# Performance work log

Hardware: AMD Instinct MI355X
Metric: run time of the kernel (lower is better)

The kernel has to match this reference:

```python
import jax, jax.numpy as jnp
import numpy as np
import math

D_MODEL = 1024
NUM_HEADS = 16
HEAD_DIM = D_MODEL // NUM_HEADS
REPETITIONS = 3
NEG = -10000.0


def setup_inputs() -> dict:
    key = jax.random.key(0)
    ks = jax.random.split(key, 5)
    B, S = 2, 2048
    x = jax.random.normal(ks[0], (B, S, D_MODEL), dtype=jnp.float32)
    Wqkv_w = jax.random.normal(ks[1], (3 * D_MODEL, D_MODEL), dtype=jnp.float32) * (1.0 / math.sqrt(D_MODEL))
    Wqkv_b = jax.random.normal(ks[2], (3 * D_MODEL,), dtype=jnp.float32) * 0.02
    out_w = jax.random.normal(ks[3], (D_MODEL, D_MODEL), dtype=jnp.float32) * (1.0 / math.sqrt(D_MODEL))
    out_b = jax.random.normal(ks[4], (D_MODEL,), dtype=jnp.float32) * 0.02
    return {"x": x, "Wqkv_w": Wqkv_w, "Wqkv_b": Wqkv_b, "out_w": out_w, "out_b": out_b}


def _self_attention(q, k, v, mask):
    # q,k,v: (B,S,H,D); mask: (S,S) additive causal (-10000 above diagonal)
    scale = 1.0 / math.sqrt(q.shape[-1])
    scores = jnp.einsum('bthd,bshd->bhts', q, k * scale) + mask  # (B,H,S,S)
    attn = jax.nn.softmax(scores, axis=-1)
    return jnp.einsum('bhts,bshd->bthd', attn, v)  # (B,S,H,D)


def reference(x, Wqkv_w, Wqkv_b, out_w, out_b):
    B, S, _ = x.shape
    qkv = x @ Wqkv_w.T + Wqkv_b                       # (B,S,3*D_MODEL)
    qkv = qkv.reshape(B, S, 3, NUM_HEADS, HEAD_DIM)
    q, k, v = qkv[:, :, 0], qkv[:, :, 1], qkv[:, :, 2]
    mask = jnp.triu(jnp.full((S, S), NEG, dtype=x.dtype), 1)
    context = _self_attention(q, k, v, mask)
    # recurrent re-attention: rep_dim == 'q' -> query replaced by previous context
    for _ in range(REPETITIONS - 1):
        context = _self_attention(context, k, v, mask)
    out = context.reshape(B, S, D_MODEL) @ out_w.T + out_b
    return out
```

## Files before the change

kernel.cpp:

```cpp
#include <hip/hip_runtime.h>


#define D_MODEL 1024
#define NHEADS  16
#define HD      64
#define SEQ     2048
#define BATCH   2
#define NROWS   (BATCH*SEQ)
#define NQKV    (3*D_MODEL)
#define SCL2F   0.1803368801111601f
#define MASK2   (-14426.950408889634f)

typedef __bf16 bf16x8 __attribute__((ext_vector_type(8)));
typedef float  f32x4  __attribute__((ext_vector_type(4)));
typedef unsigned short us8 __attribute__((ext_vector_type(8)));
typedef unsigned short us4 __attribute__((ext_vector_type(4)));
typedef short  s16x4  __attribute__((ext_vector_type(4)));

__device__ __forceinline__ unsigned short f2bf(float f) {
  unsigned int u = __float_as_uint(f);
  u = (u + 0x7fffu + ((u >> 16) & 1u)) >> 16;
  return (unsigned short)u;
}

union Pack8 { us8 v; unsigned short e[8]; };
union Pack4 { us4 v; unsigned short e[4]; };

__device__ __forceinline__ us8 cvt8(const float4 &a, const float4 &b) {
  Pack8 p;
  p.e[0]=f2bf(a.x); p.e[1]=f2bf(a.y); p.e[2]=f2bf(a.z); p.e[3]=f2bf(a.w);
  p.e[4]=f2bf(b.x); p.e[5]=f2bf(b.y); p.e[6]=f2bf(b.z); p.e[7]=f2bf(b.w);
  return p.v;
}

__device__ __forceinline__ void gl_lds16(const unsigned short* g, unsigned short* l) {
  __builtin_amdgcn_global_load_lds(
      (const __attribute__((address_space(1))) unsigned int*)g,
      (__attribute__((address_space(3))) unsigned int*)l, 16, 0, 0);
}

#define CVT_N1 (NROWS*D_MODEL)
#define CVT_N2 (NQKV*D_MODEL)
#define CVT_N3 (D_MODEL*D_MODEL)

__global__ __launch_bounds__(256) void cvt_all(
    const float* __restrict__ x, const float* __restrict__ wq,
    const float* __restrict__ ow,
    unsigned short* __restrict__ xb, unsigned short* __restrict__ wqb,
    unsigned short* __restrict__ owb)
{
  size_t i = ((size_t)blockIdx.x * 256 + threadIdx.x) * 8;
  const float* src; unsigned short* dst; size_t off;
  if (i < CVT_N1)                { src = x;  dst = xb;  off = i; }
  else if (i < CVT_N1 + CVT_N2)  { src = wq; dst = wqb; off = i - CVT_N1; }
  else                           { src = ow; dst = owb; off = i - CVT_N1 - CVT_N2; }
  float4 a = *(const float4*)(src + off);
  float4 b = *(const float4*)(src + off + 4);
  *(us8*)(dst + off) = cvt8(a, b);
}

__global__ __launch_bounds__(256) void qkv_gemm(
    const unsigned short* __restrict__ xb, const unsigned short* __restrict__ wqb,
    const float* __restrict__ bias,
    unsigned short* __restrict__ q, unsigned short* __restrict__ k,
    unsigned short* __restrict__ vT)
{
  __shared__ __align__(16) unsigned short As[128*64];
  __shared__ __align__(16) unsigned short Bs[128*64];
  const int tid = threadIdx.x;
  const int m0 = blockIdx.y * 128, n0 = blockIdx.x * 128;
  const int wave = tid >> 6, lane = tid & 63;
  const int wm = (wave >> 1) * 64, wn = (wave & 1) * 64;
  const int lrow = lane & 15, quad = lane >> 4;

  const int dr = lane >> 3;
  const int pg = lane & 7;
  const int sg = (pg ^ dr) * 8;
  const unsigned short* gA[4]; const unsigned short* gB[4];
  unsigned short *lA[4], *lB[4];
  #pragma unroll
  for (int i = 0; i < 4; i++) {
    int c = wave*4 + i;
    gA[i] = xb  + (size_t)(m0 + c*8 + dr) * D_MODEL + sg;
    gB[i] = wqb + (size_t)(n0 + c*8 + dr) * D_MODEL + sg;
    lA[i] = &As[c*512];
    lB[i] = &Bs[c*512];
  }
  const int px0 = (quad ^ (lrow & 7)) * 8;
  const int px1 = ((quad + 4) ^ (lrow & 7)) * 8;

  f32x4 acc[4][4];
  #pragma unroll
  for (int i = 0; i < 4; i++)
    #pragma unroll
    for (int j = 0; j < 4; j++) acc[i][j] = (f32x4){0.f,0.f,0.f,0.f};

  for (int k0 = 0; k0 < D_MODEL; k0 += 64) {
    __syncthreads();
    #pragma unroll
    for (int i = 0; i < 4; i++) { gl_lds16(gA[i] + k0, lA[i]); gl_lds16(gB[i] + k0, lB[i]); }
    __syncthreads();
    bf16x8 af[4][2], bfr[4][2];
    #pragma unroll
    for (int mf = 0; mf < 4; mf++) {
      int row = wm + mf*16 + lrow;
      af[mf][0] = *(const bf16x8*)&As[row*64 + px0];
      af[mf][1] = *(const bf16x8*)&As[row*64 + px1];
    }
    #pragma unroll
    for (int nb = 0; nb < 4; nb++) {
      int row = wn + nb*16 + lrow;
      bfr[nb][0] = *(const bf16x8*)&Bs[row*64 + px0];
      bfr[nb][1] = *(const bf16x8*)&Bs[row*64 + px1];
    }
    #pragma unroll
    for (int h = 0; h < 2; h++)
      #pragma unroll
      for (int mf = 0; mf < 4; mf++)
        #pragma unroll
        for (int nb = 0; nb < 4; nb++)
          acc[mf][nb] = __builtin_amdgcn_mfma_f32_16x16x32_bf16(af[mf][h], bfr[nb][h], acc[mf][nb], 0, 0, 0);
  }

  #pragma unroll
  for (int mf = 0; mf < 4; mf++) {
    #pragma unroll
    for (int nb = 0; nb < 4; nb++) {
      int n = n0 + wn + nb*16 + lrow;
      int which = n >> 10;
      int h  = (n >> 6) & 15;
      int hd = n & 63;
      int mb = m0 + wm + mf*16 + quad*4;
      int b  = mb >> 11;
      int s  = mb & 2047;
      float bi = bias[n];
      if (which == 2) {
        Pack4 p4;
        #pragma unroll
        for (int r = 0; r < 4; r++) p4.e[r] = f2bf(acc[mf][nb][r] + bi);
        *(us4*)&vT[((size_t)((b*NHEADS + h)*HD + hd))*SEQ + s] = p4.v;
      } else {
        unsigned short* dst = (which == 0) ? q : k;
        float scl = (which == 0) ? SCL2F : 1.0f;
        #pragma unroll
        for (int r = 0; r < 4; r++)
          dst[(size_t)((b*NHEADS + h)*SEQ + s + r)*HD + hd] = f2bf((acc[mf][nb][r] + bi) * scl);
      }
    }
  }
}

#define LDQ 72

__global__ __launch_bounds__(256) void attn3(
    const unsigned short* __restrict__ qg,
    const unsigned short* __restrict__ kg,
    const unsigned short* __restrict__ vTg,
    unsigned short* __restrict__ ctx)
{
  __shared__ __align__(16) unsigned short Ks[4][64*LDQ];
  __shared__ __align__(16) unsigned short Vs[4][64*LDQ];
  unsigned short* QC = &Vs[0][0];

  const int tid  = threadIdx.x;
  const int w    = tid >> 6, lane = tid & 63;
  const int lrow = lane & 15, quad = lane >> 4;
  const int bh = blockIdx.x;
  const int yy = blockIdx.y;
  const int base = (blockIdx.x + yy) & 7;
  const int qt = (yy < 8) ? base : (15 - base);
  const unsigned short* qbase = qg  + (size_t)bh * SEQ * HD;
  const unsigned short* kbase = kg  + (size_t)bh * SEQ * HD;
  const unsigned short* vbase = vTg + (size_t)bh * HD * SEQ;
  unsigned short* cbase = ctx + (size_t)bh * SEQ * HD;

  const int srow = tid >> 2;
  const int sco  = (tid & 3) * 16;
  const int qrow = tid >> 1, qc0 = (tid & 1) * 32;

  {
    const unsigned short* src = qbase + (size_t)(qt*128 + qrow)*HD + qc0;
    *(uint4*)&QC[qrow*LDQ + qc0]      = *(const uint4*)src;
    *(uint4*)&QC[qrow*LDQ + qc0 + 8]  = *(const uint4*)(src + 8);
    *(uint4*)&QC[qrow*LDQ + qc0 + 16] = *(const uint4*)(src + 16);
    *(uint4*)&QC[qrow*LDQ + qc0 + 24] = *(const uint4*)(src + 24);
  }
  __syncthreads();

  bf16x8 qb[2][2];
  #pragma unroll
  for (int qgi = 0; qgi < 2; qgi++) {
    qb[qgi][0] = *(const bf16x8*)&QC[(w*32 + qgi*16 + lrow)*LDQ + quad*8];
    qb[qgi][1] = *(const bf16x8*)&QC[(w*32 + qgi*16 + lrow)*LDQ + 32 + quad*8];
  }
  __syncthreads();

  const int qwbase = qt*128 + w*32;
  const int npair = qt + 1;

  for (int rep = 0; rep < 3; ++rep) {
    f32x4 od[2][4];
    #pragma unroll
    for (int qgi = 0; qgi < 2; qgi++)
      #pragma unroll
      for (int df = 0; df < 4; df++) od[qgi][df] = (f32x4){0.f,0.f,0.f,0.f};
    float ls[2] = {0.f, 0.f};

    uint4 ka0, ka1, kb0, kb1, va0, va1, vb0, vb1;
    {
      const unsigned short* ks = kbase + (size_t)srow*HD + sco;
      ka0 = *(const uint4*)ks;  ka1 = *(const uint4*)(ks + 8);
      kb0 = *(const uint4*)(ks + 64*HD);  kb1 = *(const uint4*)(ks + 64*HD + 8);
      const unsigned short* vs = vbase + (size_t)srow*SEQ + sco;
      va0 = *(const uint4*)vs;  va1 = *(const uint4*)(vs + 8);
      vb0 = *(const uint4*)(vs + 64);  vb1 = *(const uint4*)(vs + 64 + 8);
    }

    for (int t = 0; t < npair; ++t) {
      const int pb = (t & 1) * 2;
      *(uint4*)&Ks[pb][srow*LDQ + sco]       = ka0;
      *(uint4*)&Ks[pb][srow*LDQ + sco + 8]   = ka1;
      *(uint4*)&Ks[pb+1][srow*LDQ + sco]     = kb0;
      *(uint4*)&Ks[pb+1][srow*LDQ + sco + 8] = kb1;
      *(uint4*)&Vs[pb][srow*LDQ + sco]       = va0;
      *(uint4*)&Vs[pb][srow*LDQ + sco + 8]   = va1;
      *(uint4*)&Vs[pb+1][srow*LDQ + sco]     = vb0;
      *(uint4*)&Vs[pb+1][srow*LDQ + sco + 8] = vb1;
      if (t + 1 < npair) {
        const unsigned short* ks = kbase + (size_t)((2*t+2)*64 + srow)*HD + sco;
        ka0 = *(const uint4*)ks;  ka1 = *(const uint4*)(ks + 8);
        kb0 = *(const uint4*)(ks + 64*HD);  kb1 = *(const uint4*)(ks + 64*HD + 8);
        const unsigned short* vs = vbase + (size_t)srow*SEQ + (2*t+2)*64 + sco;
        va0 = *(const uint4*)vs;  va1 = *(const uint4*)(vs + 8);
        vb0 = *(const uint4*)(vs + 64);  vb1 = *(const uint4*)(vs + 64 + 8);
      }
      __syncthreads();

      #pragma unroll
      for (int half = 0; half < 2; ++half) {
        const int bb = pb + half;
        const int sbase = (2*t + half) * 64;
        if (sbase > qwbase + 31) continue;
        f32x4 sc[2][4];
        #pragma unroll
        for (int sf = 0; sf < 4; sf++) {
          bf16x8 a0 = *(const bf16x8*)&Ks[bb][(sf*16 + lrow)*LDQ + quad*8];
          bf16x8 a1 = *(const bf16x8*)&Ks[bb][(sf*16 + lrow)*LDQ + 32 + quad*8];
          f32x4 z0 = (f32x4){0.f,0.f,0.f,0.f}, z1 = z0;
          z0 = __builtin_amdgcn_mfma_f32_16x16x32_bf16(a0, qb[0][0], z0, 0, 0, 0);
          z1 = __builtin_amdgcn_mfma_f32_16x16x32_bf16(a0, qb[1][0], z1, 0, 0, 0);
          z0 = __builtin_amdgcn_mfma_f32_16x16x32_bf16(a1, qb[0][1], z0, 0, 0, 0);
          z1 = __builtin_amdgcn_mfma_f32_16x16x32_bf16(a1, qb[1][1], z1, 0, 0, 0);
          sc[0][sf] = z0; sc[1][sf] = z1;
        }
        if (sbase + 63 > qwbase) {
          #pragma unroll
          for (int qgi = 0; qgi < 2; qgi++) {
            int ql = qwbase + qgi*16 + lrow;
            #pragma unroll
            for (int sf = 0; sf < 4; sf++)
              #pragma unroll
              for (int r = 0; r < 4; r++)
                if (sbase + sf*16 + quad*4 + r > ql) sc[qgi][sf][r] += MASK2;
          }
        }
        s16x4 pf[2][4];
        #pragma unroll
        for (int qgi = 0; qgi < 2; qgi++) {
          float lp = 0.f;
          #pragma unroll
          for (int sf = 0; sf < 4; sf++) {
            Pack4 pk;
            #pragma unroll
            for (int r = 0; r < 4; r++) {
              float pe = __builtin_amdgcn_exp2f(sc[qgi][sf][r]);
              lp += pe;
              pk.e[r] = __builtin_bit_cast(unsigned short, (__bf16)pe);
            }
            pf[qgi][sf] = __builtin_bit_cast(s16x4, pk.v);
          }
          ls[qgi] += lp;
        }
        #pragma unroll
        for (int df = 0; df < 4; df++) {
          s16x4 v0 = *(const s16x4*)&Vs[bb][(df*16 + lrow)*LDQ +  0 + quad*4];
          s16x4 v1 = *(const s16x4*)&Vs[bb][(df*16 + lrow)*LDQ + 16 + quad*4];
          s16x4 v2 = *(const s16x4*)&Vs[bb][(df*16 + lrow)*LDQ + 32 + quad*4];
          s16x4 v3 = *(const s16x4*)&Vs[bb][(df*16 + lrow)*LDQ + 48 + quad*4];
          od[0][df] = __builtin_amdgcn_mfma_f32_16x16x16bf16_1k(v0, pf[0][0], od[0][df], 0, 0, 0);
          od[1][df] = __builtin_amdgcn_mfma_f32_16x16x16bf16_1k(v0, pf[1][0], od[1][df], 0, 0, 0);
          od[0][df] = __builtin_amdgcn_mfma_f32_16x16x16bf16_1k(v1, pf[0][1], od[0][df], 0, 0, 0);
          od[1][df] = __builtin_amdgcn_mfma_f32_16x16x16bf16_1k(v1, pf[1][1], od[1][df], 0, 0, 0);
          od[0][df] = __builtin_amdgcn_mfma_f32_16x16x16bf16_1k(v2, pf[0][2], od[0][df], 0, 0, 0);
          od[1][df] = __builtin_amdgcn_mfma_f32_16x16x16bf16_1k(v2, pf[1][2], od[1][df], 0, 0, 0);
          od[0][df] = __builtin_amdgcn_mfma_f32_16x16x16bf16_1k(v3, pf[0][3], od[0][df], 0, 0, 0);
          od[1][df] = __builtin_amdgcn_mfma_f32_16x16x16bf16_1k(v3, pf[1][3], od[1][df], 0, 0, 0);
        }
      }
    }

    #pragma unroll
    for (int qgi = 0; qgi < 2; qgi++) {
      ls[qgi] += __shfl_xor(ls[qgi], 16);
      ls[qgi] += __shfl_xor(ls[qgi], 32);
    }

    __syncthreads();
    #pragma unroll
    for (int qgi = 0; qgi < 2; qgi++) {
      float f = ((rep < 2) ? SCL2F : 1.0f) / ls[qgi];
      #pragma unroll
      for (int df = 0; df < 4; df++) {
        Pack4 pk;
        #pragma unroll
        for (int r = 0; r < 4; r++)
          pk.e[r] = __builtin_bit_cast(unsigned short, (__bf16)(od[qgi][df][r] * f));
        *(us4*)&QC[(w*32 + qgi*16 + lrow)*LDQ + df*16 + quad*4] = pk.v;
      }
    }
    __syncthreads();
    if (rep < 2) {
      #pragma unroll
      for (int qgi = 0; qgi < 2; qgi++) {
        qb[qgi][0] = *(const bf16x8*)&QC[(w*32 + qgi*16 + lrow)*LDQ + quad*8];
        qb[qgi][1] = *(const bf16x8*)&QC[(w*32 + qgi*16 + lrow)*LDQ + 32 + quad*8];
      }
      __syncthreads();
    }
  }

  {
    unsigned short* dst = cbase + (size_t)(qt*128 + qrow)*HD + qc0;
    *(uint4*)dst        = *(const uint4*)&QC[qrow*LDQ + qc0];
    *(uint4*)(dst + 8)  = *(const uint4*)&QC[qrow*LDQ + qc0 + 8];
    *(uint4*)(dst + 16) = *(const uint4*)&QC[qrow*LDQ + qc0 + 16];
    *(uint4*)(dst + 24) = *(const uint4*)&QC[qrow*LDQ + qc0 + 24];
  }
}

__global__ __launch_bounds__(256) void out_gemm(
    const unsigned short* __restrict__ ctx, const unsigned short* __restrict__ owb,
    const float* __restrict__ bias, float* __restrict__ out)
{
  __shared__ __align__(16) unsigned short As[128*64];
  __shared__ __align__(16) unsigned short Bs[64*64];
  const int tid = threadIdx.x;
  const int m0 = blockIdx.y * 128, n0 = blockIdx.x * 64;
  const int wave = tid >> 6, lane = tid & 63;
  const int wm = (wave >> 1) * 64, wn = (wave & 1) * 32;
  const int lrow = lane & 15, quad = lane >> 4;

  const int dr = lane >> 3, pg = lane & 7;
  const int sg = (pg ^ dr) * 8;
  size_t aoff[4]; unsigned short* lA[4];
  #pragma unroll
  for (int i = 0; i < 4; i++) {
    int c = wave*4 + i;
    int row = m0 + c*8 + dr;
    aoff[i] = ((size_t)((row >> 11)*NHEADS)*SEQ + (row & 2047))*HD + sg;
    lA[i] = &As[c*512];
  }
  const unsigned short* gB[2]; unsigned short* lB[2];
  #pragma unroll
  for (int j = 0; j < 2; j++) {
    int c = wave*2 + j;
    gB[j] = owb + (size_t)(n0 + c*8 + dr) * D_MODEL + sg;
    lB[j] = &Bs[c*512];
  }
  const int px0 = (quad ^ (lrow & 7)) * 8;
  const int px1 = ((quad + 4) ^ (lrow & 7)) * 8;

  f32x4 acc[4][2];
  #pragma unroll
  for (int i = 0; i < 4; i++)
    #pragma unroll
    for (int j = 0; j < 2; j++) acc[i][j] = (f32x4){0.f,0.f,0.f,0.f};

  for (int k0 = 0; k0 < D_MODEL; k0 += 64) {
    size_t hoff = (size_t)(k0 >> 6) * SEQ * HD;
    __syncthreads();
    #pragma unroll
    for (int i = 0; i < 4; i++) gl_lds16(ctx + aoff[i] + hoff, lA[i]);
    #pragma unroll
    for (int j = 0; j < 2; j++) gl_lds16(gB[j] + k0, lB[j]);
    __syncthreads();
    bf16x8 af[4][2], bfr[2][2];
    #pragma unroll
    for (int mf = 0; mf < 4; mf++) {
      int row = wm + mf*16 + lrow;
      af[mf][0] = *(const bf16x8*)&As[row*64 + px0];
      af[mf][1] = *(const bf16x8*)&As[row*64 + px1];
    }
    #pragma unroll
    for (int nb = 0; nb < 2; nb++) {
      int row = wn + nb*16 + lrow;
      bfr[nb][0] = *(const bf16x8*)&Bs[row*64 + px0];
      bfr[nb][1] = *(const bf16x8*)&Bs[row*64 + px1];
    }
    #pragma unroll
    for (int h = 0; h < 2; h++)
      #pragma unroll
      for (int mf = 0; mf < 4; mf++)
        #pragma unroll
        for (int nb = 0; nb < 2; nb++)
          acc[mf][nb] = __builtin_amdgcn_mfma_f32_16x16x32_bf16(af[mf][h], bfr[nb][h], acc[mf][nb], 0, 0, 0);
  }

  #pragma unroll
  for (int mf = 0; mf < 4; mf++) {
    #pragma unroll
    for (int nb = 0; nb < 2; nb++) {
      #pragma unroll
      for (int r = 0; r < 4; r++) {
        int mm = m0 + wm + mf*16 + quad*4 + r;
        int n  = n0 + wn + nb*16 + lrow;
        out[(size_t)mm * D_MODEL + n] = acc[mf][nb][r] + bias[n];
      }
    }
  }
}

extern "C" void kernel_launch(void* const* d_in, const int* in_sizes, int n_in,
                              void* d_out, int out_size, void* d_ws, size_t ws_size,
                              hipStream_t stream) {
  (void)in_sizes; (void)n_in; (void)out_size; (void)ws_size;
  const float* x      = (const float*)d_in[0];
  const float* Wqkv_w = (const float*)d_in[1];
  const float* Wqkv_b = (const float*)d_in[2];
  const float* out_w  = (const float*)d_in[3];
  const float* out_b  = (const float*)d_in[4];
  float* out = (float*)d_out;

  unsigned short* ws = (unsigned short*)d_ws;
  unsigned short* xb  = ws;
  unsigned short* wqb = ws + CVT_N1;
  unsigned short* owb = ws + CVT_N1 + CVT_N2;
  unsigned short* q   = ws + CVT_N1 + CVT_N2 + CVT_N3;
  unsigned short* k   = q + (size_t)NROWS*D_MODEL;
  unsigned short* vT  = k + (size_t)NROWS*D_MODEL;
  unsigned short* ctx = xb;

  cvt_all<<<(CVT_N1+CVT_N2+CVT_N3)/(256*8), 256, 0, stream>>>(x, Wqkv_w, out_w, xb, wqb, owb);
  qkv_gemm<<<dim3(NQKV/128, NROWS/128), 256, 0, stream>>>(xb, wqb, Wqkv_b, q, k, vT);
  attn3<<<dim3(BATCH*NHEADS, SEQ/128), 256, 0, stream>>>(q, k, vT, ctx);
  out_gemm<<<dim3(D_MODEL/64, NROWS/128), 256, 0, stream>>>(ctx, owb, out_b, out);
}
```

Measured before the change: 244.6 us.

## Software-pipeline attention loop to overlap QK scores with softmax and PV

Restructures the causal attention inner loop so the QK score MFMAs for the next 64-key block are issued while the softmax exp and PV MFMAs of the current block are in flight. Global-to-LDS staging of the next tile pair moves to the middle of the iteration. The diagonal block is peeled into a separate epilogue where masking is applied only there, with warps choosing the half by index. This removes per-iteration mask and skip branches but raises register pressure from holding two score tiles and depends on the peeled-tail logic being correct.

```diff
diff --git a/kernel.cpp b/kernel.cpp
--- a/kernel.cpp
+++ b/kernel.cpp
@@ -152,6 +152,60 @@
 
 #define LDQ 72
 
+__device__ __forceinline__ void qk_scores(const unsigned short* K, const bf16x8 (&qb)[2][2],
+                                          int lrow, int quad, f32x4 (&sc)[2][4]) {
+  #pragma unroll
+  for (int sf = 0; sf < 4; sf++) {
+    bf16x8 a0 = *(const bf16x8*)&K[(sf*16 + lrow)*LDQ + quad*8];
+    bf16x8 a1 = *(const bf16x8*)&K[(sf*16 + lrow)*LDQ + 32 + quad*8];
+    f32x4 z0 = (f32x4){0.f,0.f,0.f,0.f}, z1 = (f32x4){0.f,0.f,0.f,0.f};
+    z0 = __builtin_amdgcn_mfma_f32_16x16x32_bf16(a0, qb[0][0], z0, 0, 0, 0);
+    z1 = __builtin_amdgcn_mfma_f32_16x16x32_bf16(a0, qb[1][0], z1, 0, 0, 0);
+    z0 = __builtin_amdgcn_mfma_f32_16x16x32_bf16(a1, qb[0][1], z0, 0, 0, 0);
+    z1 = __builtin_amdgcn_mfma_f32_16x16x32_bf16(a1, qb[1][1], z1, 0, 0, 0);
+    sc[0][sf] = z0; sc[1][sf] = z1;
+  }
+}
+
+__device__ __forceinline__ void softmax_pf(const f32x4 (&sc)[2][4], s16x4 (&pf)[2][4],
+                                           float (&ls)[2]) {
+  #pragma unroll
+  for (int qgi = 0; qgi < 2; qgi++) {
+    float lp = 0.f;
+    #pragma unroll
+    for (int sf = 0; sf < 4; sf++) {
+      Pack4 pk;
+      #pragma unroll
+      for (int r = 0; r < 4; r++) {
+        float pe = __builtin_amdgcn_exp2f(sc[qgi][sf][r]);
+        lp += pe;
+        pk.e[r] = __builtin_bit_cast(unsigned short, (__bf16)pe);
+      }
+      pf[qgi][sf] = __builtin_bit_cast(s16x4, pk.v);
+    }
+    ls[qgi] += lp;
+  }
+}
+
+__device__ __forceinline__ void pv_accum(const unsigned short* V, const s16x4 (&pf)[2][4],
+                                         int lrow, int quad, f32x4 (&od)[2][4]) {
+  #pragma unroll
+  for (int df = 0; df < 4; df++) {
+    s16x4 v0 = *(const s16x4*)&V[(df*16 + lrow)*LDQ +  0 + quad*4];
+    s16x4 v1 = *(const s16x4*)&V[(df*16 + lrow)*LDQ + 16 + quad*4];
+    s16x4 v2 = *(const s16x4*)&V[(df*16 + lrow)*LDQ + 32 + quad*4];
+    s16x4 v3 = *(const s16x4*)&V[(df*16 + lrow)*LDQ + 48 + quad*4];
+    od[0][df] = __builtin_amdgcn_mfma_f32_16x16x16bf16_1k(v0, pf[0][0], od[0][df], 0, 0, 0);
+    od[1][df] = __builtin_amdgcn_mfma_f32_16x16x16bf16_1k(v0, pf[1][0], od[1][df], 0, 0, 0);
+    od[0][df] = __builtin_amdgcn_mfma_f32_16x16x16bf16_1k(v1, pf[0][1], od[0][df], 0, 0, 0);
+    od[1][df] = __builtin_amdgcn_mfma_f32_16x16x16bf16_1k(v1, pf[1][1], od[1][df], 0, 0, 0);
+    od[0][df] = __builtin_amdgcn_mfma_f32_16x16x16bf16_1k(v2, pf[0][2], od[0][df], 0, 0, 0);
+    od[1][df] = __builtin_amdgcn_mfma_f32_16x16x16bf16_1k(v2, pf[1][2], od[1][df], 0, 0, 0);
+    od[0][df] = __builtin_amdgcn_mfma_f32_16x16x16bf16_1k(v3, pf[0][3], od[0][df], 0, 0, 0);
+    od[1][df] = __builtin_amdgcn_mfma_f32_16x16x16bf16_1k(v3, pf[1][3], od[1][df], 0, 0, 0);
+  }
+}
+
 __global__ __launch_bounds__(256) void attn3(
     const unsigned short* __restrict__ qg,
     const unsigned short* __restrict__ kg,
@@ -215,87 +269,97 @@
       va0 = *(const uint4*)vs;  va1 = *(const uint4*)(vs + 8);
       vb0 = *(const uint4*)(vs + 64);  vb1 = *(const uint4*)(vs + 64 + 8);
     }
-
-    for (int t = 0; t < npair; ++t) {
-      const int pb = (t & 1) * 2;
-      *(uint4*)&Ks[pb][srow*LDQ + sco]       = ka0;
-      *(uint4*)&Ks[pb][srow*LDQ + sco + 8]   = ka1;
-      *(uint4*)&Ks[pb+1][srow*LDQ + sco]     = kb0;
-      *(uint4*)&Ks[pb+1][srow*LDQ + sco + 8] = kb1;
-      *(uint4*)&Vs[pb][srow*LDQ + sco]       = va0;
-      *(uint4*)&Vs[pb][srow*LDQ + sco + 8]   = va1;
-      *(uint4*)&Vs[pb+1][srow*LDQ + sco]     = vb0;
-      *(uint4*)&Vs[pb+1][srow*LDQ + sco + 8] = vb1;
-      if (t + 1 < npair) {
-        const unsigned short* ks = kbase + (size_t)((2*t+2)*64 + srow)*HD + sco;
+    *(uint4*)&Ks[0][srow*LDQ + sco]     = ka0;
+    *(uint4*)&Ks[0][srow*LDQ + sco + 8] = ka1;
+    *(uint4*)&Ks[1][srow*LDQ + sco]     = kb0;
+    *(uint4*)&Ks[1][srow*LDQ + sco + 8] = kb1;
+    *(uint4*)&Vs[0][srow*LDQ + sco]     = va0;
+    *(uint4*)&Vs[0][srow*LDQ + sco + 8] = va1;
+    *(uint4*)&Vs[1][srow*LDQ + sco]     = vb0;
+    *(uint4*)&Vs[1][srow*LDQ + sco + 8] = vb1;
+    {
+      int pt = (npair > 1) ? 2 : 0;
+      const unsigned short* ks = kbase + (size_t)(pt*64 + srow)*HD + sco;
+      ka0 = *(const uint4*)ks;  ka1 = *(const uint4*)(ks + 8);
+      kb0 = *(const uint4*)(ks + 64*HD);  kb1 = *(const uint4*)(ks + 64*HD + 8);
+      const unsigned short* vs = vbase + (size_t)srow*SEQ + pt*64 + sco;
+      va0 = *(const uint4*)vs;  va1 = *(const uint4*)(vs + 8);
+      vb0 = *(const uint4*)(vs + 64);  vb1 = *(const uint4*)(vs + 64 + 8);
+    }
+    __syncthreads();
+
+    f32x4 sc[2][4];
+    qk_scores(&Ks[0][0], qb, lrow, quad, sc);
+
+    for (int t = 0; t < npair - 1; ++t) {
+      const int pb  = (t & 1) * 2;
+      const int npb = pb ^ 2;
+
+      s16x4 pf0[2][4];
+      softmax_pf(sc, pf0, ls);
+      f32x4 sc2[2][4];
+      qk_scores(&Ks[pb+1][0], qb, lrow, quad, sc2);
+      pv_accum(&Vs[pb][0], pf0, lrow, quad, od);
+
+      s16x4 pf1[2][4];
+      softmax_pf(sc2, pf1, ls);
+      *(uint4*)&Ks[npb][srow*LDQ + sco]       = ka0;
+      *(uint4*)&Ks[npb][srow*LDQ + sco + 8]   = ka1;
+      *(uint4*)&Ks[npb+1][srow*LDQ + sco]     = kb0;
+      *(uint4*)&Ks[npb+1][srow*LDQ + sco + 8] = kb1;
+      *(uint4*)&Vs[npb][srow*LDQ + sco]       = va0;
+      *(uint4*)&Vs[npb][srow*LDQ + sco + 8]   = va1;
+      *(uint4*)&Vs[npb+1][srow*LDQ + sco]     = vb0;
+      *(uint4*)&Vs[npb+1][srow*LDQ + sco + 8] = vb1;
+      {
+        int pt2 = (t + 2 < npair) ? (2*t + 4) : 0;
+        const unsigned short* ks = kbase + (size_t)(pt2*64 + srow)*HD + sco;
         ka0 = *(const uint4*)ks;  ka1 = *(const uint4*)(ks + 8);
         kb0 = *(const uint4*)(ks + 64*HD);  kb1 = *(const uint4*)(ks + 64*HD + 8);
-        const unsigned short* vs = vbase + (size_t)srow*SEQ + (2*t+2)*64 + sco;
+        const unsigned short* vs = vbase + (size_t)srow*SEQ + pt2*64 + sco;
         va0 = *(const uint4*)vs;  va1 = *(const uint4*)(vs + 8);
         vb0 = *(const uint4*)(vs + 64);  vb1 = *(const uint4*)(vs + 64 + 8);
       }
+      pv_accum(&Vs[pb+1][0], pf1, lrow, quad, od);
+
       __syncthreads();
-
-      #pragma unroll
-      for (int half = 0; half < 2; ++half) {
-        const int bb = pb + half;
-        const int sbase = (2*t + half) * 64;
-        if (sbase > qwbase + 31) continue;
-        f32x4 sc[2][4];
-        #pragma unroll
-        for (int sf = 0; sf < 4; sf++) {
-          bf16x8 a0 = *(const bf16x8*)&Ks[bb][(sf*16 + lrow)*LDQ + quad*8];
-          bf16x8 a1 = *(const bf16x8*)&Ks[bb][(sf*16 + lrow)*LDQ + 32 + quad*8];
-          f32x4 z0 = (f32x4){0.f,0.f,0.f,0.f}, z1 = z0;
-          z0 = __builtin_amdgcn_mfma_f32_16x16x32_bf16(a0, qb[0][0], z0, 0, 0, 0);
-          z1 = __builtin_amdgcn_mfma_f32_16x16x32_bf16(a0, qb[1][0], z1, 0, 0, 0);
-          z0 = __builtin_amdgcn_mfma_f32_16x16x32_bf16(a1, qb[0][1], z0, 0, 0, 0);
-          z1 = __builtin_amdgcn_mfma_f32_16x16x32_bf16(a1, qb[1][1], z1, 0, 0, 0);
-          sc[0][sf] = z0; sc[1][sf] = z1;
+      qk_scores(&Ks[npb][0], qb, lrow, quad, sc);
+    }
+
+    {
+      const int pb = ((npair - 1) & 1) * 2;
+      const int sbase0 = (npair - 1) * 128;
+      if (w < 2) {
+        #pragma unroll
+        for (int qgi = 0; qgi < 2; qgi++) {
+          int ql = qwbase + qgi*16 + lrow;
+          #pragma unroll
+          for (int sf = 0; sf < 4; sf++)
+            #pragma unroll
+            for (int r = 0; r < 4; r++)
+              if (sbase0 + sf*16 + quad*4 + r > ql) sc[qgi][sf][r] += MASK2;
         }
-        if (sbase + 63 > qwbase) {
+      }
+      s16x4 pf0[2][4];
+      softmax_pf(sc, pf0, ls);
+      pv_accum(&Vs[pb][0], pf0, lrow, quad, od);
+
+      if (w >= 2) {
+        f32x4 sc2[2][4];
+        qk_scores(&Ks[pb+1][0], qb, lrow, quad, sc2);
+        const int sbase1 = sbase0 + 64;
+        #pragma unroll
+        for (int qgi = 0; qgi < 2; qgi++) {
+          int ql = qwbase + qgi*16 + lrow;
           #pragma unroll
-          for (int qgi = 0; qgi < 2; qgi++) {
-            int ql = qwbase + qgi*16 + lrow;
+          for (int sf = 0; sf < 4; sf++)
             #pragma unroll
-            for (int sf = 0; sf < 4; sf++)
-              #pragma unroll
-              for (int r = 0; r < 4; r++)
-                if (sbase + sf*16 + quad*4 + r > ql) sc[qgi][sf][r] += MASK2;
-          }
+            for (int r = 0; r < 4; r++)
+              if (sbase1 + sf*16 + quad*4 + r > ql) sc2[qgi][sf][r] += MASK2;
         }
-        s16x4 pf[2][4];
-        #pragma unroll
-        for (int qgi = 0; qgi < 2; qgi++) {
-          float lp = 0.f;
-          #pragma unroll
-          for (int sf = 0; sf < 4; sf++) {
-            Pack4 pk;
-            #pragma unroll
-            for (int r = 0; r < 4; r++) {
-              float pe = __builtin_amdgcn_exp2f(sc[qgi][sf][r]);
-              lp += pe;
-              pk.e[r] = __builtin_bit_cast(unsigned short, (__bf16)pe);
-            }
-            pf[qgi][sf] = __builtin_bit_cast(s16x4, pk.v);
-          }
-          ls[qgi] += lp;
-        }
-        #pragma unroll
-        for (int df = 0; df < 4; df++) {
-          s16x4 v0 = *(const s16x4*)&Vs[bb][(df*16 + lrow)*LDQ +  0 + quad*4];
-          s16x4 v1 = *(const s16x4*)&Vs[bb][(df*16 + lrow)*LDQ + 16 + quad*4];
-          s16x4 v2 = *(const s16x4*)&Vs[bb][(df*16 + lrow)*LDQ + 32 + quad*4];
-          s16x4 v3 = *(const s16x4*)&Vs[bb][(df*16 + lrow)*LDQ + 48 + quad*4];
-          od[0][df] = __builtin_amdgcn_mfma_f32_16x16x16bf16_1k(v0, pf[0][0], od[0][df], 0, 0, 0);
-          od[1][df] = __builtin_amdgcn_mfma_f32_16x16x16bf16_1k(v0, pf[1][0], od[1][df], 0, 0, 0);
-          od[0][df] = __builtin_amdgcn_mfma_f32_16x16x16bf16_1k(v1, pf[0][1], od[0][df], 0, 0, 0);
-          od[1][df] = __builtin_amdgcn_mfma_f32_16x16x16bf16_1k(v1, pf[1][1], od[1][df], 0, 0, 0);
-          od[0][df] = __builtin_amdgcn_mfma_f32_16x16x16bf16_1k(v2, pf[0][2], od[0][df], 0, 0, 0);
-          od[1][df] = __builtin_amdgcn_mfma_f32_16x16x16bf16_1k(v2, pf[1][2], od[1][df], 0, 0, 0);
-          od[0][df] = __builtin_amdgcn_mfma_f32_16x16x16bf16_1k(v3, pf[0][3], od[0][df], 0, 0, 0);
-          od[1][df] = __builtin_amdgcn_mfma_f32_16x16x16bf16_1k(v3, pf[1][3], od[1][df], 0, 0, 0);
-        }
+        s16x4 pf1[2][4];
+        softmax_pf(sc2, pf1, ls);
+        pv_accum(&Vs[pb+1][0], pf1, lrow, quad, od);
       }
     }
 
```

New measurement: 276.6 us. 13.1% more time.

## Use 512-thread attention blocks covering 256 query rows with MFMA priority hints

Applied to the files above, without the earlier changes.

The attention kernel now launches 512-thread blocks, each handling 256 query rows with 8 waves, so every K/V tile loaded into shared memory serves twice as many queries. The per-thread K/V staging is halved to match. The grid drops to 8 query tiles per head and the balanced causal tile remapping is removed, so block work is uneven again. s_setprio hints are placed around the MFMA sections so waves doing matrix work get issue priority. Risks include worse load balance from the causal skew, fewer blocks, and a 2-blocks-per-CU occupancy target at 512 threads.

```diff
diff --git a/kernel.cpp b/kernel.cpp
--- a/kernel.cpp
+++ b/kernel.cpp
@@ -152,7 +152,7 @@
 
 #define LDQ 72
 
-__global__ __launch_bounds__(256) void attn3(
+__global__ __launch_bounds__(512, 2) void attn3(
     const unsigned short* __restrict__ qg,
     const unsigned short* __restrict__ kg,
     const unsigned short* __restrict__ vTg,
@@ -165,21 +165,19 @@
   const int tid  = threadIdx.x;
   const int w    = tid >> 6, lane = tid & 63;
   const int lrow = lane & 15, quad = lane >> 4;
-  const int bh = blockIdx.x;
-  const int yy = blockIdx.y;
-  const int base = (blockIdx.x + yy) & 7;
-  const int qt = (yy < 8) ? base : (15 - base);
+  const int bh  = blockIdx.x;
+  const int qt8 = blockIdx.y;
   const unsigned short* qbase = qg  + (size_t)bh * SEQ * HD;
   const unsigned short* kbase = kg  + (size_t)bh * SEQ * HD;
   const unsigned short* vbase = vTg + (size_t)bh * HD * SEQ;
   unsigned short* cbase = ctx + (size_t)bh * SEQ * HD;
 
-  const int srow = tid >> 2;
-  const int sco  = (tid & 3) * 16;
+  const int srow = tid >> 3;
+  const int sco  = (tid & 7) * 8;
   const int qrow = tid >> 1, qc0 = (tid & 1) * 32;
 
   {
-    const unsigned short* src = qbase + (size_t)(qt*128 + qrow)*HD + qc0;
+    const unsigned short* src = qbase + (size_t)(qt8*256 + qrow)*HD + qc0;
     *(uint4*)&QC[qrow*LDQ + qc0]      = *(const uint4*)src;
     *(uint4*)&QC[qrow*LDQ + qc0 + 8]  = *(const uint4*)(src + 8);
     *(uint4*)&QC[qrow*LDQ + qc0 + 16] = *(const uint4*)(src + 16);
@@ -195,8 +193,8 @@
   }
   __syncthreads();
 
-  const int qwbase = qt*128 + w*32;
-  const int npair = qt + 1;
+  const int qwbase = qt8*256 + w*32;
+  const int npair = 2*qt8 + 2;
 
   for (int rep = 0; rep < 3; ++rep) {
     f32x4 od[2][4];
@@ -206,33 +204,25 @@
       for (int df = 0; df < 4; df++) od[qgi][df] = (f32x4){0.f,0.f,0.f,0.f};
     float ls[2] = {0.f, 0.f};
 
-    uint4 ka0, ka1, kb0, kb1, va0, va1, vb0, vb1;
+    uint4 ka, kb, va, vb;
     {
       const unsigned short* ks = kbase + (size_t)srow*HD + sco;
-      ka0 = *(const uint4*)ks;  ka1 = *(const uint4*)(ks + 8);
-      kb0 = *(const uint4*)(ks + 64*HD);  kb1 = *(const uint4*)(ks + 64*HD + 8);
+      ka = *(const uint4*)ks;  kb = *(const uint4*)(ks + 64*HD);
       const unsigned short* vs = vbase + (size_t)srow*SEQ + sco;
-      va0 = *(const uint4*)vs;  va1 = *(const uint4*)(vs + 8);
-      vb0 = *(const uint4*)(vs + 64);  vb1 = *(const uint4*)(vs + 64 + 8);
+      va = *(const uint4*)vs;  vb = *(const uint4*)(vs + 64);
     }
 
     for (int t = 0; t < npair; ++t) {
       const int pb = (t & 1) * 2;
-      *(uint4*)&Ks[pb][srow*LDQ + sco]       = ka0;
-      *(uint4*)&Ks[pb][srow*LDQ + sco + 8]   = ka1;
-      *(uint4*)&Ks[pb+1][srow*LDQ + sco]     = kb0;
-      *(uint4*)&Ks[pb+1][srow*LDQ + sco + 8] = kb1;
-      *(uint4*)&Vs[pb][srow*LDQ + sco]       = va0;
-      *(uint4*)&Vs[pb][srow*LDQ + sco + 8]   = va1;
-      *(uint4*)&Vs[pb+1][srow*LDQ + sco]     = vb0;
-      *(uint4*)&Vs[pb+1][srow*LDQ + sco + 8] = vb1;
+      *(uint4*)&Ks[pb][srow*LDQ + sco]   = ka;
+      *(uint4*)&Ks[pb+1][srow*LDQ + sco] = kb;
+      *(uint4*)&Vs[pb][srow*LDQ + sco]   = va;
+      *(uint4*)&Vs[pb+1][srow*LDQ + sco] = vb;
       if (t + 1 < npair) {
         const unsigned short* ks = kbase + (size_t)((2*t+2)*64 + srow)*HD + sco;
-        ka0 = *(const uint4*)ks;  ka1 = *(const uint4*)(ks + 8);
-        kb0 = *(const uint4*)(ks + 64*HD);  kb1 = *(const uint4*)(ks + 64*HD + 8);
+        ka = *(const uint4*)ks;  kb = *(const uint4*)(ks + 64*HD);
         const unsigned short* vs = vbase + (size_t)srow*SEQ + (2*t+2)*64 + sco;
-        va0 = *(const uint4*)vs;  va1 = *(const uint4*)(vs + 8);
-        vb0 = *(const uint4*)(vs + 64);  vb1 = *(const uint4*)(vs + 64 + 8);
+        va = *(const uint4*)vs;  vb = *(const uint4*)(vs + 64);
       }
       __syncthreads();
 
@@ -242,17 +232,19 @@
         const int sbase = (2*t + half) * 64;
         if (sbase > qwbase + 31) continue;
         f32x4 sc[2][4];
+        __builtin_amdgcn_s_setprio(1);
         #pragma unroll
         for (int sf = 0; sf < 4; sf++) {
           bf16x8 a0 = *(const bf16x8*)&Ks[bb][(sf*16 + lrow)*LDQ + quad*8];
           bf16x8 a1 = *(const bf16x8*)&Ks[bb][(sf*16 + lrow)*LDQ + 32 + quad*8];
-          f32x4 z0 = (f32x4){0.f,0.f,0.f,0.f}, z1 = z0;
+          f32x4 z0 = (f32x4){0.f,0.f,0.f,0.f}, z1 = (f32x4){0.f,0.f,0.f,0.f};
           z0 = __builtin_amdgcn_mfma_f32_16x16x32_bf16(a0, qb[0][0], z0, 0, 0, 0);
           z1 = __builtin_amdgcn_mfma_f32_16x16x32_bf16(a0, qb[1][0], z1, 0, 0, 0);
           z0 = __builtin_amdgcn_mfma_f32_16x16x32_bf16(a1, qb[0][1], z0, 0, 0, 0);
           z1 = __builtin_amdgcn_mfma_f32_16x16x32_bf16(a1, qb[1][1], z1, 0, 0, 0);
           sc[0][sf] = z0; sc[1][sf] = z1;
         }
+        __builtin_amdgcn_s_setprio(0);
         if (sbase + 63 > qwbase) {
           #pragma unroll
           for (int qgi = 0; qgi < 2; qgi++) {
@@ -281,6 +273,7 @@
           }
           ls[qgi] += lp;
         }
+        __builtin_amdgcn_s_setprio(1);
         #pragma unroll
         for (int df = 0; df < 4; df++) {
           s16x4 v0 = *(const s16x4*)&Vs[bb][(df*16 + lrow)*LDQ +  0 + quad*4];
@@ -296,6 +289,7 @@
           od[0][df] = __builtin_amdgcn_mfma_f32_16x16x16bf16_1k(v3, pf[0][3], od[0][df], 0, 0, 0);
           od[1][df] = __builtin_amdgcn_mfma_f32_16x16x16bf16_1k(v3, pf[1][3], od[1][df], 0, 0, 0);
         }
+        __builtin_amdgcn_s_setprio(0);
       }
     }
 
@@ -330,7 +324,7 @@
   }
 
   {
-    unsigned short* dst = cbase + (size_t)(qt*128 + qrow)*HD + qc0;
+    unsigned short* dst = cbase + (size_t)(qt8*256 + qrow)*HD + qc0;
     *(uint4*)dst        = *(const uint4*)&QC[qrow*LDQ + qc0];
     *(uint4*)(dst + 8)  = *(const uint4*)&QC[qrow*LDQ + qc0 + 8];
     *(uint4*)(dst + 16) = *(const uint4*)&QC[qrow*LDQ + qc0 + 16];
@@ -442,6 +436,6 @@
 
   cvt_all<<<(CVT_N1+CVT_N2+CVT_N3)/(256*8), 256, 0, stream>>>(x, Wqkv_w, out_w, xb, wqb, owb);
   qkv_gemm<<<dim3(NQKV/128, NROWS/128), 256, 0, stream>>>(xb, wqb, Wqkv_b, q, k, vT);
-  attn3<<<dim3(BATCH*NHEADS, SEQ/128), 256, 0, stream>>>(q, k, vT, ctx);
+  attn3<<<dim3(BATCH*NHEADS, 8), 512, 0, stream>>>(q, k, vT, ctx);
   out_gemm<<<dim3(D_MODEL/64, NROWS/128), 256, 0, stream>>>(ctx, owb, out_b, out);
 }
```

Measured after the change: 262.0 us. +7.1%, slower.
